# Optimization experiments

Hardware: AMD Instinct MI355X
Metric: run time of the kernel (lower is better)

## Reference

```python
import jax, jax.numpy as jnp
import numpy as np

B, T, S, H, V, L = 2048, 48, 128, 256, 96, 2


def setup_inputs() -> dict:
    key = jax.random.key(0)
    ks = jax.random.split(key, 16)
    s = 0.05
    y = jax.random.randint(ks[0], (B, T), 0, V)
    encoder_outputs = jax.random.normal(ks[1], (B, S, H), jnp.float32)
    encoder_hidden = jax.random.normal(ks[2], (L, B, H), jnp.float32)
    params = {
        'W_ih0': jax.random.normal(ks[3], (3 * H, V + H), jnp.float32) * s,
        'W_hh0': jax.random.normal(ks[4], (3 * H, H), jnp.float32) * s,
        'b_ih0': jax.random.normal(ks[5], (3 * H,), jnp.float32) * s,
        'b_hh0': jax.random.normal(ks[6], (3 * H,), jnp.float32) * s,
        'W_ih1': jax.random.normal(ks[7], (3 * H, H), jnp.float32) * s,
        'W_hh1': jax.random.normal(ks[8], (3 * H, H), jnp.float32) * s,
        'b_ih1': jax.random.normal(ks[9], (3 * H,), jnp.float32) * s,
        'b_hh1': jax.random.normal(ks[10], (3 * H,), jnp.float32) * s,
        'wc_W': jax.random.normal(ks[11], (H, 2 * H), jnp.float32) * s,
        'wc_b': jax.random.normal(ks[12], (H,), jnp.float32) * s,
        'ws_W': jax.random.normal(ks[13], (V, H), jnp.float32) * s,
        'ws_b': jax.random.normal(ks[14], (V,), jnp.float32) * s,
    }
    return dict(y=y, encoder_outputs=encoder_outputs, encoder_hidden=encoder_hidden,
                is_training=1, **params)


def _gru_cell(x, h, Wih, Whh, bih, bhh):
    # PyTorch GRUCell math
    gi = x @ Wih.T + bih
    gh = h @ Whh.T + bhh
    ir, iz, inn = jnp.split(gi, 3, axis=-1)
    hr, hz, hn = jnp.split(gh, 3, axis=-1)
    r = jax.nn.sigmoid(ir + hr)
    z = jax.nn.sigmoid(iz + hz)
    n = jnp.tanh(inn + r * hn)
    return (1.0 - z) * n + z * h


def reference(y, encoder_outputs, encoder_hidden, is_training,
              W_ih0, W_hh0, b_ih0, b_hh0, W_ih1, W_hh1, b_ih1, b_hh1,
              wc_W, wc_b, ws_W, ws_b):
    # Teacher-forcing (is_training=True) path; embedding is fixed one-hot.
    vocab = ws_W.shape[0]
    xs = jax.nn.one_hot(y[:, :-1], vocab, dtype=encoder_outputs.dtype)  # [B,T-1,V]
    xs = jnp.swapaxes(xs, 0, 1)  # [T-1,B,V]
    h0, h1 = encoder_hidden[0], encoder_hidden[1]
    last_ht = jnp.zeros_like(h0)

    def step(carry, x_t):
        lht, c0, c1 = carry
        rnn_in = jnp.concatenate([x_t, lht], axis=-1)  # [B, V+H]
        c0n = _gru_cell(rnn_in, c0, W_ih0, W_hh0, b_ih0, b_hh0)
        c1n = _gru_cell(c0n, c1, W_ih1, W_hh1, b_ih1, b_hh1)
        out = c1n  # GRU top-layer output, [B,H]
        energy = jnp.einsum('bsh,bh->bs', encoder_outputs, out)
        alpha = jax.nn.softmax(energy, axis=-1)
        ctx = jnp.einsum('bs,bsh->bh', alpha, encoder_outputs)
        ht = jnp.tanh(jnp.concatenate([out, ctx], axis=-1) @ wc_W.T + wc_b)
        logits = ht @ ws_W.T + ws_b  # [B,V]
        return (ht, c0n, c1n), logits

    _, outs = jax.lax.scan(step, (last_ht, h0, h1), xs)
    return jnp.swapaxes(outs, 0, 1)  # [B, T-1, V]
```

## Files before the change

### kernel.cpp

```cpp
#include <hip/hip_runtime.h>

#define BATCH 2048
#define TTOT 48
#define TOUT 47
#define SS 128
#define HH 256
#define VV 96
#define MB 8
#define NBLK (BATCH / MB)
#define NTHR 512
#define SROW 260

#define OFF_T0I 0
#define OFF_T0H 196608
#define OFF_T1I 393216
#define OFF_T1H 589824
#define OFF_TG  786432
#define OFF_TC  860160
#define OFF_TS  991232
#define WS_FLOATS 1015808

struct __align__(16) SMem {
    float htF[MB * SROW];
    float c0F[MB * SROW];
    float c1F[MB * SROW];
    float cxF[MB * SROW];
    float gI[MB * 768];
    float gH[MB * 768];
    float gI2[MB * 768];
    float gH2[MB * 768];
    int   ymS[MB];
};

__device__ __forceinline__ float dot4(const float4 a, const float4 b) {
    return a.x * b.x + a.y * b.y + a.z * b.z + a.w * b.w;
}

__device__ __forceinline__ void gru_gemv2(
    const float* __restrict__ TI, const float* __restrict__ TH,
    const float* __restrict__ bih, const float* __restrict__ bhh,
    const float* xS, const float* hS,
    float* gI, float* gH, float* gI2, float* gH2, const int tid)
{
    const int kh = tid >> 8;
    const int i0 = tid & 255;
    const float* __restrict__ bI = TI + (size_t)kh * 98304;
    const float* __restrict__ bH = TH + (size_t)kh * 98304;
    float aI0[MB], aI1[MB], aI2[MB], aH0[MB], aH1[MB], aH2[MB];
    const float bi0 = kh ? 0.f : bih[i0];
    const float bi1 = kh ? 0.f : bih[i0 + 256];
    const float bi2 = kh ? 0.f : bih[i0 + 512];
    const float bh0 = kh ? 0.f : bhh[i0];
    const float bh1 = kh ? 0.f : bhh[i0 + 256];
    const float bh2 = kh ? 0.f : bhh[i0 + 512];
    #pragma unroll
    for (int m = 0; m < MB; ++m) {
        aI0[m] = bi0; aI1[m] = bi1; aI2[m] = bi2;
        aH0[m] = bh0; aH1[m] = bh1; aH2[m] = bh2;
    }
    const float* xk = xS + kh * 128;
    const float* hk = hS + kh * 128;
    #pragma unroll 2
    for (int kk = 0; kk < 32; ++kk) {
        const float4 wi0 = *(const float4*)(bI + ((size_t)kk * 768 + i0) * 4);
        const float4 wi1 = *(const float4*)(bI + ((size_t)kk * 768 + i0 + 256) * 4);
        const float4 wi2 = *(const float4*)(bI + ((size_t)kk * 768 + i0 + 512) * 4);
        const float4 wh0 = *(const float4*)(bH + ((size_t)kk * 768 + i0) * 4);
        const float4 wh1 = *(const float4*)(bH + ((size_t)kk * 768 + i0 + 256) * 4);
        const float4 wh2 = *(const float4*)(bH + ((size_t)kk * 768 + i0 + 512) * 4);
        #pragma unroll
        for (int m = 0; m < MB; ++m) {
            const float4 x4 = *(const float4*)(xk + m * SROW + kk * 4);
            const float4 h4 = *(const float4*)(hk + m * SROW + kk * 4);
            aI0[m] += dot4(wi0, x4); aI1[m] += dot4(wi1, x4); aI2[m] += dot4(wi2, x4);
            aH0[m] += dot4(wh0, h4); aH1[m] += dot4(wh1, h4); aH2[m] += dot4(wh2, h4);
        }
    }
    float* dI = kh ? gI2 : gI;
    float* dH = kh ? gH2 : gH;
    #pragma unroll
    for (int m = 0; m < MB; ++m) {
        dI[m * 768 + i0]       = aI0[m];
        dI[m * 768 + i0 + 256] = aI1[m];
        dI[m * 768 + i0 + 512] = aI2[m];
        dH[m * 768 + i0]       = aH0[m];
        dH[m * 768 + i0 + 256] = aH1[m];
        dH[m * 768 + i0 + 512] = aH2[m];
    }
}

__global__ __launch_bounds__(NTHR, 2) void decoder_kernel(
    const int* __restrict__ y,
    const float* __restrict__ enc,
    const float* __restrict__ eh,
    const float* __restrict__ bih0,
    const float* __restrict__ bhh0,
    const float* __restrict__ bih1,
    const float* __restrict__ bhh1,
    const float* __restrict__ wcb,
    const float* __restrict__ wsb,
    const float* __restrict__ ws,
    float* __restrict__ out)
{
    __shared__ SMem sm;
    const int tid = threadIdx.x;
    const int b0 = blockIdx.x * MB;

    const float* __restrict__ T0I = ws + OFF_T0I;
    const float* __restrict__ T0H = ws + OFF_T0H;
    const float* __restrict__ T1I = ws + OFF_T1I;
    const float* __restrict__ T1H = ws + OFF_T1H;
    const float* __restrict__ TG  = ws + OFF_TG;
    const float* __restrict__ TC  = ws + OFF_TC;
    const float* __restrict__ TS  = ws + OFF_TS;

    for (int idx = tid; idx < MB * SROW; idx += NTHR) sm.htF[idx] = 0.f;
    for (int idx = tid; idx < MB * HH; idx += NTHR) {
        const int m = idx >> 8, k = idx & 255;
        sm.c0F[m * SROW + k] = eh[(b0 + m) * HH + k];
        sm.c1F[m * SROW + k] = eh[(size_t)BATCH * HH + (b0 + m) * HH + k];
    }
    __syncthreads();

    for (int t = 0; t < TOUT; ++t) {
        if (tid < MB) sm.ymS[tid] = y[(b0 + tid) * TTOT + t];

        gru_gemv2(T0I, T0H, bih0, bhh0, sm.htF, sm.c0F,
                  sm.gI, sm.gH, sm.gI2, sm.gH2, tid);
        __syncthreads();
        for (int p = tid; p < MB * 256; p += NTHR) {
            const int m = p >> 8, c = p & 255;
            const float* tg = TG + (size_t)sm.ymS[m] * 768;
            const float giR = sm.gI[m * 768 + c]       + sm.gI2[m * 768 + c]       + tg[c];
            const float ghR = sm.gH[m * 768 + c]       + sm.gH2[m * 768 + c];
            const float giZ = sm.gI[m * 768 + 256 + c] + sm.gI2[m * 768 + 256 + c] + tg[256 + c];
            const float ghZ = sm.gH[m * 768 + 256 + c] + sm.gH2[m * 768 + 256 + c];
            const float giN = sm.gI[m * 768 + 512 + c] + sm.gI2[m * 768 + 512 + c] + tg[512 + c];
            const float ghN = sm.gH[m * 768 + 512 + c] + sm.gH2[m * 768 + 512 + c];
            const float r = 1.f / (1.f + __expf(-(giR + ghR)));
            const float z = 1.f / (1.f + __expf(-(giZ + ghZ)));
            const float n = tanhf(giN + r * ghN);
            sm.c0F[m * SROW + c] = (1.f - z) * n + z * sm.c0F[m * SROW + c];
        }
        __syncthreads();

        gru_gemv2(T1I, T1H, bih1, bhh1, sm.c0F, sm.c1F,
                  sm.gI, sm.gH, sm.gI2, sm.gH2, tid);
        __syncthreads();
        for (int p = tid; p < MB * 256; p += NTHR) {
            const int m = p >> 8, c = p & 255;
            const float giR = sm.gI[m * 768 + c]       + sm.gI2[m * 768 + c];
            const float ghR = sm.gH[m * 768 + c]       + sm.gH2[m * 768 + c];
            const float giZ = sm.gI[m * 768 + 256 + c] + sm.gI2[m * 768 + 256 + c];
            const float ghZ = sm.gH[m * 768 + 256 + c] + sm.gH2[m * 768 + 256 + c];
            const float giN = sm.gI[m * 768 + 512 + c] + sm.gI2[m * 768 + 512 + c];
            const float ghN = sm.gH[m * 768 + 512 + c] + sm.gH2[m * 768 + 512 + c];
            const float r = 1.f / (1.f + __expf(-(giR + ghR)));
            const float z = 1.f / (1.f + __expf(-(giZ + ghZ)));
            const float n = tanhf(giN + r * ghN);
            sm.c1F[m * SROW + c] = (1.f - z) * n + z * sm.c1F[m * SROW + c];
        }
        __syncthreads();

        {
            const int m = tid >> 6, lane = tid & 63;
            const float4 o4 = *(const float4*)(sm.c1F + m * SROW + lane * 4);
            const float* er = enc + (size_t)(b0 + m) * SS * HH + lane * 4;
            float4 C = {0.f, 0.f, 0.f, 0.f};
            float D = 0.f, Mx = -3.0e38f;
            for (int s = 0; s < SS; s += 2) {
                const float4 a4 = *(const float4*)(er);
                const float4 b4 = *(const float4*)(er + HH);
                er += 2 * HH;
                float e0 = dot4(a4, o4);
                float e1 = dot4(b4, o4);
                #pragma unroll
                for (int off = 1; off < 64; off <<= 1) {
                    e0 += __shfl_xor(e0, off);
                    e1 += __shfl_xor(e1, off);
                }
                const float nm = fmaxf(Mx, fmaxf(e0, e1));
                const float sc = __expf(Mx - nm);
                const float p0 = __expf(e0 - nm);
                const float p1 = __expf(e1 - nm);
                D = D * sc + p0 + p1;
                C.x = C.x * sc + p0 * a4.x + p1 * b4.x;
                C.y = C.y * sc + p0 * a4.y + p1 * b4.y;
                C.z = C.z * sc + p0 * a4.z + p1 * b4.z;
                C.w = C.w * sc + p0 * a4.w + p1 * b4.w;
                Mx = nm;
            }
            const float inv = 1.f / D;
            float4 cx;
            cx.x = C.x * inv; cx.y = C.y * inv; cx.z = C.z * inv; cx.w = C.w * inv;
            *(float4*)(sm.cxF + m * SROW + lane * 4) = cx;
        }
        __syncthreads();

        {
            const int i0w = tid & 127;
            const int sel = (tid >> 7) & 1;
            const int khf = tid >> 8;
            const float* st = (sel ? sm.cxF : sm.c1F) + khf * 128;
            const float* base = TC + ((size_t)sel * 64 * 256 + (size_t)khf * 32 * 256) * 4;
            float a0[MB], a1[MB];
            #pragma unroll
            for (int m = 0; m < MB; ++m) { a0[m] = 0.f; a1[m] = 0.f; }
            #pragma unroll 2
            for (int kk = 0; kk < 32; ++kk) {
                const float4 w0 = *(const float4*)(base + ((size_t)kk * 256 + i0w) * 4);
                const float4 w1 = *(const float4*)(base + ((size_t)kk * 256 + i0w + 128) * 4);
                #pragma unroll
                for (int m = 0; m < MB; ++m) {
                    const float4 s4 = *(const float4*)(st + m * SROW + kk * 4);
                    a0[m] += dot4(w0, s4);
                    a1[m] += dot4(w1, s4);
                }
            }
            float* dst = sel ? sm.gH : sm.gI;
            #pragma unroll
            for (int m = 0; m < MB; ++m) {
                dst[m * 768 + khf * 256 + i0w]       = a0[m];
                dst[m * 768 + khf * 256 + i0w + 128] = a1[m];
            }
        }
        __syncthreads();
        for (int p = tid; p < MB * 256; p += NTHR) {
            const int m = p >> 8, i = p & 255;
            sm.htF[m * SROW + i] = tanhf(sm.gI[m * 768 + i] + sm.gI[m * 768 + 256 + i]
                                       + sm.gH[m * 768 + i] + sm.gH[m * 768 + 256 + i]
                                       + wcb[i]);
        }
        __syncthreads();

        for (int p = tid; p < MB * VV; p += NTHR) {
            const int m = p / VV, v = p - m * VV;
            const float* h = sm.htF + m * SROW;
            float acc = wsb[v];
            #pragma unroll 4
            for (int k4 = 0; k4 < 64; ++k4)
                acc += dot4(*(const float4*)(TS + ((size_t)k4 * 96 + v) * 4),
                            *(const float4*)(h + k4 * 4));
            out[(size_t)((b0 + m) * TOUT + t) * VV + v] = acc;
        }
    }
}

__global__ __launch_bounds__(256) void prep_kernel(
    const float* __restrict__ Wih0, const float* __restrict__ Whh0,
    const float* __restrict__ Wih1, const float* __restrict__ Whh1,
    const float* __restrict__ wcW,  const float* __restrict__ wsW,
    float* __restrict__ ws)
{
    const int idx = blockIdx.x * 256 + threadIdx.x;
    if (idx < OFF_T0H) {
        const int j = idx & 3, q = idx >> 2;
        const int i = q % 768, k4 = q / 768;
        ws[idx] = Wih0[i * 352 + 96 + k4 * 4 + j];
    } else if (idx < OFF_T1I) {
        const int v = idx - OFF_T0H;
        const int j = v & 3, q = v >> 2;
        const int i = q % 768, k4 = q / 768;
        ws[idx] = Whh0[i * 256 + k4 * 4 + j];
    } else if (idx < OFF_T1H) {
        const int v = idx - OFF_T1I;
        const int j = v & 3, q = v >> 2;
        const int i = q % 768, k4 = q / 768;
        ws[idx] = Wih1[i * 256 + k4 * 4 + j];
    } else if (idx < OFF_TG) {
        const int v = idx - OFF_T1H;
        const int j = v & 3, q = v >> 2;
        const int i = q % 768, k4 = q / 768;
        ws[idx] = Whh1[i * 256 + k4 * 4 + j];
    } else if (idx < OFF_TC) {
        const int v = idx - OFF_TG;
        const int col = v / 768, i = v % 768;
        ws[idx] = Wih0[i * 352 + col];
    } else if (idx < OFF_TS) {
        const int v = idx - OFF_TC;
        const int j = v & 3, q = v >> 2;
        const int i = q & 255, q2 = q >> 8;
        const int k4 = q2 & 63, sel = q2 >> 6;
        ws[idx] = wcW[i * 512 + sel * 256 + k4 * 4 + j];
    } else if (idx < WS_FLOATS) {
        const int v = idx - OFF_TS;
        const int j = v & 3, q = v >> 2;
        const int vv = q % 96, k4 = q / 96;
        ws[idx] = wsW[vv * 256 + k4 * 4 + j];
    }
}

extern "C" void kernel_launch(void* const* d_in, const int* in_sizes, int n_in,
                              void* d_out, int out_size, void* d_ws, size_t ws_size,
                              hipStream_t stream) {
    (void)in_sizes; (void)n_in; (void)out_size; (void)ws_size;
    const int* y = (const int*)d_in[0];
    const float* enc  = (const float*)d_in[1];
    const float* eh   = (const float*)d_in[2];
    const float* Wih0 = (const float*)d_in[4];
    const float* Whh0 = (const float*)d_in[5];
    const float* bih0 = (const float*)d_in[6];
    const float* bhh0 = (const float*)d_in[7];
    const float* Wih1 = (const float*)d_in[8];
    const float* Whh1 = (const float*)d_in[9];
    const float* bih1 = (const float*)d_in[10];
    const float* bhh1 = (const float*)d_in[11];
    const float* wcW  = (const float*)d_in[12];
    const float* wcb  = (const float*)d_in[13];
    const float* wsW  = (const float*)d_in[14];
    const float* wsb  = (const float*)d_in[15];
    float* outp = (float*)d_out;
    float* wsp  = (float*)d_ws;

    prep_kernel<<<dim3(WS_FLOATS / 256), dim3(256), 0, stream>>>(
        Wih0, Whh0, Wih1, Whh1, wcW, wsW, wsp);
    decoder_kernel<<<dim3(NBLK), dim3(NTHR), 0, stream>>>(
        y, enc, eh, bih0, bhh0, bih1, bhh1, wcb, wsb, wsp, outp);
}
```

Before: 8.201 ms.

## Double threads per block and split GEMV, attention and combine work across them

Raises the block to 1024 threads and splits the work so each thread does less. The GRU GEMV now gives input and hidden weights to separate thread groups, attention splits the sequence into two halves merged with an online-softmax combine, and the output projection splits the batch rows. It also swaps the shuffle reductions for DPP-based wave sums and drops the padded shared-memory row stride. Fewer accumulators per thread may ease register pressure, but there is an extra sync and merge pass, possible LDS bank conflicts, and fewer blocks can fit per CU.

```diff
diff --git a/kernel.cpp b/kernel.cpp
--- a/kernel.cpp
+++ b/kernel.cpp
@@ -8,8 +8,7 @@
 #define VV 96
 #define MB 8
 #define NBLK (BATCH / MB)
-#define NTHR 512
-#define SROW 260
+#define NTHR 1024
 
 #define OFF_T0I 0
 #define OFF_T0H 196608
@@ -21,75 +20,94 @@
 #define WS_FLOATS 1015808
 
 struct __align__(16) SMem {
-    float htF[MB * SROW];
-    float c0F[MB * SROW];
-    float c1F[MB * SROW];
-    float cxF[MB * SROW];
-    float gI[MB * 768];
-    float gH[MB * 768];
-    float gI2[MB * 768];
-    float gH2[MB * 768];
-    int   ymS[MB];
+    float ht[MB * 256];
+    float c0[MB * 256];
+    float c1[MB * 256];
+    float cx[MB * 256];
+    float g[12 * 2048];
+    float Dp[2][MB];
+    float Mp[2][MB];
+    int   ym[MB];
 };
 
 __device__ __forceinline__ float dot4(const float4 a, const float4 b) {
     return a.x * b.x + a.y * b.y + a.z * b.z + a.w * b.w;
 }
 
-__device__ __forceinline__ void gru_gemv2(
+__device__ __forceinline__ float wave_sum64(float v) {
+    v += __int_as_float(__builtin_amdgcn_update_dpp(0, __float_as_int(v), 0x111, 0xf, 0xf, true));
+    v += __int_as_float(__builtin_amdgcn_update_dpp(0, __float_as_int(v), 0x112, 0xf, 0xf, true));
+    v += __int_as_float(__builtin_amdgcn_update_dpp(0, __float_as_int(v), 0x114, 0xf, 0xf, true));
+    v += __int_as_float(__builtin_amdgcn_update_dpp(0, __float_as_int(v), 0x118, 0xf, 0xf, true));
+    v += __int_as_float(__builtin_amdgcn_update_dpp(0, __float_as_int(v), 0x142, 0xa, 0xf, true));
+    v += __int_as_float(__builtin_amdgcn_update_dpp(0, __float_as_int(v), 0x143, 0xc, 0xf, true));
+    return __int_as_float(__builtin_amdgcn_readlane(__float_as_int(v), 63));
+}
+
+__device__ __forceinline__ void gru_gemv(
     const float* __restrict__ TI, const float* __restrict__ TH,
     const float* __restrict__ bih, const float* __restrict__ bhh,
-    const float* xS, const float* hS,
-    float* gI, float* gH, float* gI2, float* gH2, const int tid)
+    const float* xS, const float* hS, float* g, const int tid)
 {
-    const int kh = tid >> 8;
+    const int kh = tid >> 9;
+    const int side = (tid >> 8) & 1;
     const int i0 = tid & 255;
-    const float* __restrict__ bI = TI + (size_t)kh * 98304;
-    const float* __restrict__ bH = TH + (size_t)kh * 98304;
-    float aI0[MB], aI1[MB], aI2[MB], aH0[MB], aH1[MB], aH2[MB];
-    const float bi0 = kh ? 0.f : bih[i0];
-    const float bi1 = kh ? 0.f : bih[i0 + 256];
-    const float bi2 = kh ? 0.f : bih[i0 + 512];
-    const float bh0 = kh ? 0.f : bhh[i0];
-    const float bh1 = kh ? 0.f : bhh[i0 + 256];
-    const float bh2 = kh ? 0.f : bhh[i0 + 512];
+    const float* __restrict__ bW = (side ? TH : TI) + (size_t)kh * 98304;
+    const float* __restrict__ bias = side ? bhh : bih;
+    const float* sk = (side ? hS : xS) + kh * 128;
+    float a0[MB], a1[MB], a2[MB];
+    const float b0v = kh ? 0.f : bias[i0];
+    const float b1v = kh ? 0.f : bias[i0 + 256];
+    const float b2v = kh ? 0.f : bias[i0 + 512];
+    #pragma unroll
+    for (int m = 0; m < MB; ++m) { a0[m] = b0v; a1[m] = b1v; a2[m] = b2v; }
+    #pragma unroll 2
+    for (int kk = 0; kk < 32; ++kk) {
+        const float4 w0 = *(const float4*)(bW + ((size_t)kk * 768 + i0) * 4);
+        const float4 w1 = *(const float4*)(bW + ((size_t)kk * 768 + i0 + 256) * 4);
+        const float4 w2 = *(const float4*)(bW + ((size_t)kk * 768 + i0 + 512) * 4);
+        #pragma unroll
+        for (int m = 0; m < MB; ++m) {
+            const float4 s4 = *(const float4*)(sk + m * 256 + kk * 4);
+            a0[m] += dot4(w0, s4);
+            a1[m] += dot4(w1, s4);
+            a2[m] += dot4(w2, s4);
+        }
+    }
+    const int cb = (kh * 2 + side) * 3 * 2048;
     #pragma unroll
     for (int m = 0; m < MB; ++m) {
-        aI0[m] = bi0; aI1[m] = bi1; aI2[m] = bi2;
-        aH0[m] = bh0; aH1[m] = bh1; aH2[m] = bh2;
-    }
-    const float* xk = xS + kh * 128;
-    const float* hk = hS + kh * 128;
-    #pragma unroll 2
-    for (int kk = 0; kk < 32; ++kk) {
-        const float4 wi0 = *(const float4*)(bI + ((size_t)kk * 768 + i0) * 4);
-        const float4 wi1 = *(const float4*)(bI + ((size_t)kk * 768 + i0 + 256) * 4);
-        const float4 wi2 = *(const float4*)(bI + ((size_t)kk * 768 + i0 + 512) * 4);
-        const float4 wh0 = *(const float4*)(bH + ((size_t)kk * 768 + i0) * 4);
-        const float4 wh1 = *(const float4*)(bH + ((size_t)kk * 768 + i0 + 256) * 4);
-        const float4 wh2 = *(const float4*)(bH + ((size_t)kk * 768 + i0 + 512) * 4);
-        #pragma unroll
-        for (int m = 0; m < MB; ++m) {
-            const float4 x4 = *(const float4*)(xk + m * SROW + kk * 4);
-            const float4 h4 = *(const float4*)(hk + m * SROW + kk * 4);
-            aI0[m] += dot4(wi0, x4); aI1[m] += dot4(wi1, x4); aI2[m] += dot4(wi2, x4);
-            aH0[m] += dot4(wh0, h4); aH1[m] += dot4(wh1, h4); aH2[m] += dot4(wh2, h4);
-        }
-    }
-    float* dI = kh ? gI2 : gI;
-    float* dH = kh ? gH2 : gH;
-    #pragma unroll
-    for (int m = 0; m < MB; ++m) {
-        dI[m * 768 + i0]       = aI0[m];
-        dI[m * 768 + i0 + 256] = aI1[m];
-        dI[m * 768 + i0 + 512] = aI2[m];
-        dH[m * 768 + i0]       = aH0[m];
-        dH[m * 768 + i0 + 256] = aH1[m];
-        dH[m * 768 + i0 + 512] = aH2[m];
-    }
-}
-
-__global__ __launch_bounds__(NTHR, 2) void decoder_kernel(
+        g[cb + m * 256 + i0]            = a0[m];
+        g[cb + 2048 + m * 256 + i0]     = a1[m];
+        g[cb + 4096 + m * 256 + i0]     = a2[m];
+    }
+}
+
+template <bool GATHER>
+__device__ __forceinline__ void gru_update(
+    const float* g, float* st, const float* __restrict__ TG, const int* ym, const int tid)
+{
+    for (int p = tid; p < MB * 256; p += NTHR) {
+        const int m = p >> 8, c = p & 255;
+        const float* gm = g + m * 256 + c;
+        float iR = gm[0 * 2048] + gm[6 * 2048];
+        float hR = gm[3 * 2048] + gm[9 * 2048];
+        float iZ = gm[1 * 2048] + gm[7 * 2048];
+        float hZ = gm[4 * 2048] + gm[10 * 2048];
+        float iN = gm[2 * 2048] + gm[8 * 2048];
+        const float hN = gm[5 * 2048] + gm[11 * 2048];
+        if (GATHER) {
+            const float* tg = TG + (size_t)ym[m] * 768;
+            iR += tg[c]; iZ += tg[256 + c]; iN += tg[512 + c];
+        }
+        const float r = 1.f / (1.f + __expf(-(iR + hR)));
+        const float z = 1.f / (1.f + __expf(-(iZ + hZ)));
+        const float n = tanhf(iN + r * hN);
+        st[p] = (1.f - z) * n + z * st[p];
+    }
+}
+
+__global__ __launch_bounds__(NTHR, 4) void decoder_kernel(
     const int* __restrict__ y,
     const float* __restrict__ enc,
     const float* __restrict__ eh,
@@ -114,71 +132,38 @@
     const float* __restrict__ TC  = ws + OFF_TC;
     const float* __restrict__ TS  = ws + OFF_TS;
 
-    for (int idx = tid; idx < MB * SROW; idx += NTHR) sm.htF[idx] = 0.f;
-    for (int idx = tid; idx < MB * HH; idx += NTHR) {
-        const int m = idx >> 8, k = idx & 255;
-        sm.c0F[m * SROW + k] = eh[(b0 + m) * HH + k];
-        sm.c1F[m * SROW + k] = eh[(size_t)BATCH * HH + (b0 + m) * HH + k];
+    for (int idx = tid; idx < MB * 256; idx += NTHR) {
+        sm.ht[idx] = 0.f;
+        sm.c0[idx] = eh[b0 * HH + idx];
+        sm.c1[idx] = eh[(size_t)BATCH * HH + b0 * HH + idx];
     }
     __syncthreads();
 
     for (int t = 0; t < TOUT; ++t) {
-        if (tid < MB) sm.ymS[tid] = y[(b0 + tid) * TTOT + t];
-
-        gru_gemv2(T0I, T0H, bih0, bhh0, sm.htF, sm.c0F,
-                  sm.gI, sm.gH, sm.gI2, sm.gH2, tid);
-        __syncthreads();
-        for (int p = tid; p < MB * 256; p += NTHR) {
-            const int m = p >> 8, c = p & 255;
-            const float* tg = TG + (size_t)sm.ymS[m] * 768;
-            const float giR = sm.gI[m * 768 + c]       + sm.gI2[m * 768 + c]       + tg[c];
-            const float ghR = sm.gH[m * 768 + c]       + sm.gH2[m * 768 + c];
-            const float giZ = sm.gI[m * 768 + 256 + c] + sm.gI2[m * 768 + 256 + c] + tg[256 + c];
-            const float ghZ = sm.gH[m * 768 + 256 + c] + sm.gH2[m * 768 + 256 + c];
-            const float giN = sm.gI[m * 768 + 512 + c] + sm.gI2[m * 768 + 512 + c] + tg[512 + c];
-            const float ghN = sm.gH[m * 768 + 512 + c] + sm.gH2[m * 768 + 512 + c];
-            const float r = 1.f / (1.f + __expf(-(giR + ghR)));
-            const float z = 1.f / (1.f + __expf(-(giZ + ghZ)));
-            const float n = tanhf(giN + r * ghN);
-            sm.c0F[m * SROW + c] = (1.f - z) * n + z * sm.c0F[m * SROW + c];
-        }
-        __syncthreads();
-
-        gru_gemv2(T1I, T1H, bih1, bhh1, sm.c0F, sm.c1F,
-                  sm.gI, sm.gH, sm.gI2, sm.gH2, tid);
-        __syncthreads();
-        for (int p = tid; p < MB * 256; p += NTHR) {
-            const int m = p >> 8, c = p & 255;
-            const float giR = sm.gI[m * 768 + c]       + sm.gI2[m * 768 + c];
-            const float ghR = sm.gH[m * 768 + c]       + sm.gH2[m * 768 + c];
-            const float giZ = sm.gI[m * 768 + 256 + c] + sm.gI2[m * 768 + 256 + c];
-            const float ghZ = sm.gH[m * 768 + 256 + c] + sm.gH2[m * 768 + 256 + c];
-            const float giN = sm.gI[m * 768 + 512 + c] + sm.gI2[m * 768 + 512 + c];
-            const float ghN = sm.gH[m * 768 + 512 + c] + sm.gH2[m * 768 + 512 + c];
-            const float r = 1.f / (1.f + __expf(-(giR + ghR)));
-            const float z = 1.f / (1.f + __expf(-(giZ + ghZ)));
-            const float n = tanhf(giN + r * ghN);
-            sm.c1F[m * SROW + c] = (1.f - z) * n + z * sm.c1F[m * SROW + c];
-        }
+        if (tid < MB) sm.ym[tid] = y[(b0 + tid) * TTOT + t];
+
+        gru_gemv(T0I, T0H, bih0, bhh0, sm.ht, sm.c0, sm.g, tid);
+        __syncthreads();
+        gru_update<true>(sm.g, sm.c0, TG, sm.ym, tid);
+        __syncthreads();
+
+        gru_gemv(T1I, T1H, bih1, bhh1, sm.c0, sm.c1, sm.g, tid);
+        __syncthreads();
+        gru_update<false>(sm.g, sm.c1, TG, sm.ym, tid);
         __syncthreads();
 
         {
-            const int m = tid >> 6, lane = tid & 63;
-            const float4 o4 = *(const float4*)(sm.c1F + m * SROW + lane * 4);
-            const float* er = enc + (size_t)(b0 + m) * SS * HH + lane * 4;
+            const int m = tid >> 7, sh = (tid >> 6) & 1, lane = tid & 63;
+            const float4 o4 = *(const float4*)(sm.c1 + m * 256 + lane * 4);
+            const float* er = enc + ((size_t)(b0 + m) * SS + sh * 64) * HH + lane * 4;
             float4 C = {0.f, 0.f, 0.f, 0.f};
             float D = 0.f, Mx = -3.0e38f;
-            for (int s = 0; s < SS; s += 2) {
+            for (int s = 0; s < 64; s += 2) {
                 const float4 a4 = *(const float4*)(er);
                 const float4 b4 = *(const float4*)(er + HH);
                 er += 2 * HH;
-                float e0 = dot4(a4, o4);
-                float e1 = dot4(b4, o4);
-                #pragma unroll
-                for (int off = 1; off < 64; off <<= 1) {
-                    e0 += __shfl_xor(e0, off);
-                    e1 += __shfl_xor(e1, off);
-                }
+                const float e0 = wave_sum64(dot4(a4, o4));
+                const float e1 = wave_sum64(dot4(b4, o4));
                 const float nm = fmaxf(Mx, fmaxf(e0, e1));
                 const float sc = __expf(Mx - nm);
                 const float p0 = __expf(e0 - nm);
@@ -190,52 +175,61 @@
                 C.w = C.w * sc + p0 * a4.w + p1 * b4.w;
                 Mx = nm;
             }
-            const float inv = 1.f / D;
-            float4 cx;
-            cx.x = C.x * inv; cx.y = C.y * inv; cx.z = C.z * inv; cx.w = C.w * inv;
-            *(float4*)(sm.cxF + m * SROW + lane * 4) = cx;
+            *(float4*)(sm.g + (sh * 8 + m) * 256 + lane * 4) = C;
+            if (lane == 0) { sm.Dp[sh][m] = D; sm.Mp[sh][m] = Mx; }
+        }
+        __syncthreads();
+        for (int p = tid; p < MB * 256; p += NTHR) {
+            const int m = p >> 8, h = p & 255;
+            const float M0 = sm.Mp[0][m], M1 = sm.Mp[1][m];
+            const float Mt = fmaxf(M0, M1);
+            const float e0 = __expf(M0 - Mt), e1 = __expf(M1 - Mt);
+            const float den = sm.Dp[0][m] * e0 + sm.Dp[1][m] * e1;
+            const float num = sm.g[m * 256 + h] * e0 + sm.g[(8 + m) * 256 + h] * e1;
+            sm.cx[p] = num / den;
         }
         __syncthreads();
 
         {
             const int i0w = tid & 127;
             const int sel = (tid >> 7) & 1;
-            const int khf = tid >> 8;
-            const float* st = (sel ? sm.cxF : sm.c1F) + khf * 128;
-            const float* base = TC + ((size_t)sel * 64 * 256 + (size_t)khf * 32 * 256) * 4;
-            float a0[MB], a1[MB];
+            const int khf = (tid >> 8) & 1;
+            const int mh  = tid >> 9;
+            const float* st = (sel ? sm.cx : sm.c1) + khf * 128;
+            const float* base = TC + ((size_t)sel * 16384 + (size_t)khf * 8192) * 4;
+            float a0[4], a1[4];
             #pragma unroll
-            for (int m = 0; m < MB; ++m) { a0[m] = 0.f; a1[m] = 0.f; }
+            for (int q = 0; q < 4; ++q) { a0[q] = 0.f; a1[q] = 0.f; }
             #pragma unroll 2
             for (int kk = 0; kk < 32; ++kk) {
                 const float4 w0 = *(const float4*)(base + ((size_t)kk * 256 + i0w) * 4);
                 const float4 w1 = *(const float4*)(base + ((size_t)kk * 256 + i0w + 128) * 4);
                 #pragma unroll
-                for (int m = 0; m < MB; ++m) {
-                    const float4 s4 = *(const float4*)(st + m * SROW + kk * 4);
-                    a0[m] += dot4(w0, s4);
-                    a1[m] += dot4(w1, s4);
+                for (int q = 0; q < 4; ++q) {
+                    const float4 s4 = *(const float4*)(st + (mh * 4 + q) * 256 + kk * 4);
+                    a0[q] += dot4(w0, s4);
+                    a1[q] += dot4(w1, s4);
                 }
             }
-            float* dst = sel ? sm.gH : sm.gI;
             #pragma unroll
-            for (int m = 0; m < MB; ++m) {
-                dst[m * 768 + khf * 256 + i0w]       = a0[m];
-                dst[m * 768 + khf * 256 + i0w + 128] = a1[m];
+            for (int q = 0; q < 4; ++q) {
+                const int m = mh * 4 + q;
+                sm.g[((sel * 2 + khf) * 8 + m) * 256 + i0w]       = a0[q];
+                sm.g[((sel * 2 + khf) * 8 + m) * 256 + i0w + 128] = a1[q];
             }
         }
         __syncthreads();
         for (int p = tid; p < MB * 256; p += NTHR) {
             const int m = p >> 8, i = p & 255;
-            sm.htF[m * SROW + i] = tanhf(sm.gI[m * 768 + i] + sm.gI[m * 768 + 256 + i]
-                                       + sm.gH[m * 768 + i] + sm.gH[m * 768 + 256 + i]
-                                       + wcb[i]);
+            sm.ht[p] = tanhf(sm.g[(0 * 8 + m) * 256 + i] + sm.g[(1 * 8 + m) * 256 + i]
+                           + sm.g[(2 * 8 + m) * 256 + i] + sm.g[(3 * 8 + m) * 256 + i]
+                           + wcb[i]);
         }
         __syncthreads();
 
         for (int p = tid; p < MB * VV; p += NTHR) {
             const int m = p / VV, v = p - m * VV;
-            const float* h = sm.htF + m * SROW;
+            const float* h = sm.ht + m * 256;
             float acc = wsb[v];
             #pragma unroll 4
             for (int k4 = 0; k4 < 64; ++k4)
```

New measurement: 6.804 ms. -17.0%, faster.
